# Optimization experiments

Hardware: AMD Instinct MI355X
Metric: run time of the kernel (lower is better)

The kernel has to match this reference:

```python
import jax, jax.numpy as jnp
import numpy as np

SEQ, BATCH, HIDDEN = 4096, 16, 512


def setup_inputs() -> dict:
    key = jax.random.key(0)
    ks = jax.random.split(key, 8)
    scale = 1.0 / np.sqrt(HIDDEN)
    outputs_hidden = jax.random.normal(ks[0], (1, BATCH, HIDDEN), jnp.float32)
    encoder_out = jax.random.normal(ks[1], (SEQ, BATCH, HIDDEN), jnp.float32)
    encoder_features = jax.random.normal(ks[2], (SEQ, BATCH, HIDDEN), jnp.float32)
    # binary-ish float mask, mostly ones
    encoder_mask = (jax.random.uniform(ks[3], (BATCH, 1, SEQ)) > 0.1).astype(jnp.float32)
    # running sum of positive exp-scores; keep strictly positive
    temporal_scores_sum = jax.random.uniform(ks[4], (BATCH, 1, SEQ)) + 0.5
    W_feat = jax.random.normal(ks[5], (HIDDEN, HIDDEN), jnp.float32) * scale
    b_feat = jax.random.normal(ks[6], (HIDDEN,), jnp.float32)
    v_attn = jax.random.normal(ks[7], (HIDDEN,), jnp.float32) * scale
    return {
        "outputs_hidden": outputs_hidden,
        "encoder_out": encoder_out,
        "encoder_features": encoder_features,
        "encoder_mask": encoder_mask,
        "temporal_scores_sum": temporal_scores_sum,
        "W_feat": W_feat,
        "b_feat": b_feat,
        "v_attn": v_attn,
    }


def reference(outputs_hidden, encoder_out, encoder_features, encoder_mask,
              temporal_scores_sum, W_feat, b_feat, v_attn):
    # self.features: Linear(hidden, hidden) on decoder state [1, b, h]
    decoder_features = jnp.einsum('obh,kh->obk', outputs_hidden, W_feat) + b_feat
    # additive score: tanh(dec + enc) . v  -> [s, b]
    scores = jnp.einsum('sbh,h->sb', jnp.tanh(decoder_features + encoder_features), v_attn)
    # Permute(1,2,0) of [s,b,1] -> [b,1,s], then exp
    temporal_attention = jnp.exp(scores).T[:, None, :]  # [b, 1, s]
    attention = temporal_attention / temporal_scores_sum
    new_scores_sum = temporal_attention + temporal_scores_sum
    attention = attention * encoder_mask
    attention = attention / jnp.sum(attention, axis=-1, keepdims=True)  # Normalize(-1)
    enc = jnp.transpose(encoder_out, (1, 0, 2))           # [b, s, h]
    context = jnp.matmul(attention, enc)                  # [b, 1, h]
    context = jnp.transpose(context, (1, 0, 2))           # [1, b, h]
    return context, attention, new_scores_sum
```

## Files before the change

kernel.cpp:

```cpp
#include <hip/hip_runtime.h>
#include <hip/hip_bf16.h>
#include <stdint.h>

#define SEQ 4096
#define BATCH 16
#define HID 512
#define ATT_OFF (BATCH * HID)
#define NSS_OFF (BATCH * HID + BATCH * SEQ)

#define SPW 2
#define NT 4
#define SBLK (4 * NT * SPW)
#define NGRP (SEQ / SBLK)
#define NBLK (BATCH * NGRP)

typedef unsigned short u16;
typedef unsigned int u32;

__device__ __forceinline__ float bflo(u32 w) { return __uint_as_float(w << 16); }
__device__ __forceinline__ float bfhi(u32 w) { return __uint_as_float(w & 0xffff0000u); }

__device__ __forceinline__ u16 f2bf(float f) {
  u32 u = __float_as_uint(f);
  return (u16)((u + 0x7fffu + ((u >> 16) & 1u)) >> 16);
}

__device__ __forceinline__ int probe_bf16(const void* tssp) {
  const u16* t = (const u16*)tssp;
  int ok = 1;
  #pragma unroll
  for (int i = 0; i < 8; i += 2) {
    u16 u = t[i];
    ok &= (u >= 0x3F00 && u <= 0x3FC0) ? 1 : 0;
  }
  return ok;
}

template <int BF>
__device__ __forceinline__ float ld1(const void* p, size_t i) {
  if (BF) return __uint_as_float(((u32)((const u16*)p)[i]) << 16);
  return ((const float*)p)[i];
}

template <int BF>
__device__ __forceinline__ void st1(void* p, size_t i, float v) {
  if (BF) ((u16*)p)[i] = f2bf(v);
  else    ((float*)p)[i] = v;
}

template <int BF>
__device__ __forceinline__ void load8(const void* p, size_t e, float* o) {
  if (BF) {
    uint4 v = *(const uint4*)((const u16*)p + e);
    o[0]=bflo(v.x); o[1]=bfhi(v.x); o[2]=bflo(v.y); o[3]=bfhi(v.y);
    o[4]=bflo(v.z); o[5]=bfhi(v.z); o[6]=bflo(v.w); o[7]=bfhi(v.w);
  } else {
    const float4* f = (const float4*)((const float*)p + e);
    float4 a = f[0], b = f[1];
    o[0]=a.x; o[1]=a.y; o[2]=a.z; o[3]=a.w;
    o[4]=b.x; o[5]=b.y; o[6]=b.z; o[7]=b.w;
  }
}

__device__ __forceinline__ float fast_tanh(float x) {
  float e = __expf(2.0f * x);
  return 1.0f - 2.0f * __builtin_amdgcn_rcpf(e + 1.0f);
}

template <int BF>
__device__ __forceinline__ void k_dec_body(
    const void* oh, const void* W, const void* bias, float* dec) {
  int tid = threadIdx.x;
  int gw = blockIdx.x * 4 + (tid >> 6);
  int lane = tid & 63;
  int k = gw & (HID - 1);
  int b = gw >> 9;
  float wv[8], ov[8];
  load8<BF>(W,  (size_t)k * HID + lane * 8, wv);
  load8<BF>(oh, (size_t)b * HID + lane * 8, ov);
  float acc = 0.0f;
  #pragma unroll
  for (int j = 0; j < 8; ++j) acc += wv[j] * ov[j];
  #pragma unroll
  for (int off = 32; off; off >>= 1) acc += __shfl_xor(acc, off, 64);
  if (lane == 0) dec[b * HID + k] = acc + ld1<BF>(bias, k);
}

__global__ __launch_bounds__(256) void k_dec(
    const void* oh, const void* W, const void* bias, const void* tss,
    float* dec, float* denom) {
  if (blockIdx.x == 0 && threadIdx.x < BATCH) denom[threadIdx.x] = 0.0f;
  if (probe_bf16(tss)) k_dec_body<1>(oh, W, bias, dec);
  else                 k_dec_body<0>(oh, W, bias, dec);
}

template <int BF>
__device__ __forceinline__ void k_str_body(
    const void* ef, const void* eo, const void* maskp, const void* tssp,
    const void* vp, const float* dec, float* w_buf, float* denom,
    float* partial, void* out) {
  int tid = threadIdx.x, lane = tid & 63, wave = tid >> 6;
  int blk = blockIdx.x;
  int b = blk & (BATCH - 1);
  int grp = blk >> 4;
  int sw = grp * SBLK + wave * (NT * SPW);

  float dv[8], vv[8];
  #pragma unroll
  for (int j = 0; j < 8; ++j) dv[j] = dec[b * HID + lane * 8 + j];
  load8<BF>(vp, lane * 8, vv);

  float evA[SPW][8], evB[SPW][8], eoA[SPW][8], eoB[SPW][8];
  float tsA[SPW], tsB[SPW], mA[SPW], mB[SPW];
  float a[8] = {0,0,0,0,0,0,0,0};
  float wsum = 0.0f;

  auto LOADT = [&](float (&ev)[SPW][8], float (&eov)[SPW][8],
                   float (&ts)[SPW], float (&m)[SPW], int t) {
    int s0 = sw + t * SPW;
    #pragma unroll
    for (int i = 0; i < SPW; ++i) {
      size_t row = ((size_t)(s0 + i) * BATCH + b) * HID + lane * 8;
      load8<BF>(ef, row, ev[i]);
      load8<BF>(eo, row, eov[i]);
    }
    #pragma unroll
    for (int i = 0; i < SPW; ++i) {
      ts[i] = ld1<BF>(tssp,  b * SEQ + s0 + i);
      m[i]  = ld1<BF>(maskp, b * SEQ + s0 + i);
    }
  };
  auto COMPT = [&](float (&ev)[SPW][8], float (&eov)[SPW][8],
                   float (&ts)[SPW], float (&m)[SPW], int t) {
    int s0 = sw + t * SPW;
    float acc[SPW];
    #pragma unroll
    for (int i = 0; i < SPW; ++i) {
      float s = 0.0f;
      #pragma unroll
      for (int j = 0; j < 8; ++j) s += fast_tanh(ev[i][j] + dv[j]) * vv[j];
      acc[i] = s;
    }
    #pragma unroll
    for (int off = 32; off; off >>= 1) {
      #pragma unroll
      for (int i = 0; i < SPW; ++i) acc[i] += __shfl_xor(acc[i], off, 64);
    }
    #pragma unroll
    for (int i = 0; i < SPW; ++i) {
      float p  = __expf(acc[i]);
      float wv = p * m[i] * __builtin_amdgcn_rcpf(ts[i]);
      wsum += wv;
      if (lane == 0) {
        st1<BF>(out, NSS_OFF + b * SEQ + s0 + i, p + ts[i]);
        w_buf[b * SEQ + s0 + i] = wv;
      }
      #pragma unroll
      for (int j = 0; j < 8; ++j) a[j] += wv * eov[i][j];
    }
  };

  LOADT(evA, eoA, tsA, mA, 0);
  LOADT(evB, eoB, tsB, mB, 1);
  COMPT(evA, eoA, tsA, mA, 0);  LOADT(evA, eoA, tsA, mA, 2);
  COMPT(evB, eoB, tsB, mB, 1);  LOADT(evB, eoB, tsB, mB, 3);
  COMPT(evA, eoA, tsA, mA, 2);
  COMPT(evB, eoB, tsB, mB, 3);

  __shared__ float red[3 * 8 * 64];
  __shared__ float wpart[4];
  if (lane == 0) wpart[wave] = wsum;
  if (wave > 0) {
    #pragma unroll
    for (int j = 0; j < 8; ++j) red[((wave - 1) * 8 + j) * 64 + lane] = a[j];
  }
  __syncthreads();
  if (wave == 0) {
    #pragma unroll
    for (int k = 0; k < 3; ++k)
      #pragma unroll
      for (int j = 0; j < 8; ++j) a[j] += red[(k * 8 + j) * 64 + lane];
    float4* p4 = (float4*)(partial + ((size_t)b * NGRP + grp) * HID + lane * 8);
    p4[0] = make_float4(a[0], a[1], a[2], a[3]);
    p4[1] = make_float4(a[4], a[5], a[6], a[7]);
    if (tid == 0)
      atomicAdd(&denom[b], wpart[0] + wpart[1] + wpart[2] + wpart[3]);
  }
}

__global__ __launch_bounds__(256, 3) void k_str(
    const void* ef, const void* eo, const void* maskp, const void* tssp,
    const void* vp, const float* dec, float* w_buf, float* denom,
    float* partial, void* out) {
  if (probe_bf16(tssp))
    k_str_body<1>(ef, eo, maskp, tssp, vp, dec, w_buf, denom, partial, out);
  else
    k_str_body<0>(ef, eo, maskp, tssp, vp, dec, w_buf, denom, partial, out);
}

template <int BF>
__device__ __forceinline__ void k_fin_body(
    const float* w_buf, const float* denom, const float* partial, void* out) {
  int b = blockIdx.x >> 5;
  int part = blockIdx.x & 31;
  int t = threadIdx.x;
  float inv_d = __builtin_amdgcn_rcpf(denom[b]);
  if (t < 128) {
    int s = part * 128 + t;
    st1<BF>(out, ATT_OFF + b * SEQ + s, w_buf[b * SEQ + s] * inv_d);
  }
  int hl = t >> 4, cp = t & 15;
  int h = part * 16 + hl;
  float sum = 0.0f;
  #pragma unroll
  for (int c = cp; c < NGRP; c += 16)
    sum += partial[((size_t)b * NGRP + c) * HID + h];
  #pragma unroll
  for (int off = 8; off; off >>= 1) sum += __shfl_xor(sum, off, 64);
  if (cp == 0) st1<BF>(out, b * HID + h, sum * inv_d);
}

__global__ __launch_bounds__(256) void k_finalize(
    const float* w_buf, const float* denom, const float* partial,
    const void* tssp, void* out) {
  if (probe_bf16(tssp)) k_fin_body<1>(w_buf, denom, partial, out);
  else                  k_fin_body<0>(w_buf, denom, partial, out);
}

extern "C" void kernel_launch(void* const* d_in, const int* in_sizes, int n_in,
                              void* d_out, int out_size, void* d_ws, size_t ws_size,
                              hipStream_t stream) {
  const void* oh   = d_in[0];
  const void* eo   = d_in[1];
  const void* ef   = d_in[2];
  const void* mask = d_in[3];
  const void* tss  = d_in[4];
  const void* W    = d_in[5];
  const void* bias = d_in[6];
  const void* v    = d_in[7];

  float* ws      = (float*)d_ws;
  float* dec     = ws;
  float* w_buf   = dec + BATCH * HID;
  float* denom   = w_buf + BATCH * SEQ;
  float* partial = denom + 16;

  k_dec     <<<2048, 256, 0, stream>>>(oh, W, bias, tss, dec, denom);
  k_str     <<<NBLK, 256, 0, stream>>>(ef, eo, mask, tss, v, dec, w_buf,
                                       denom, partial, d_out);
  k_finalize<<< 512, 256, 0, stream>>>(w_buf, denom, partial, tss, d_out);
}
```

Measured before the change: 293.8 us.

## Replace register double-buffered streaming with simple loop and raise occupancy

Removes the manual two-slot software pipelining of encoder rows in the streaming kernel and uses a plain non-unrolled loop over 8 sequence positions per wave. Register pressure drops, so the launch bound asks for 8 blocks per CU instead of 3, relying on more resident waves to hide memory latency instead of explicit prefetch. The per-block sequence chunk shrinks from 32 to 32 rows (same SBLK), so the grid and the partial layout stay unchanged. The risk is less memory-level parallelism per wave if the scheduler cannot cover the load latency.

```diff
diff --git a/kernel.cpp b/kernel.cpp
--- a/kernel.cpp
+++ b/kernel.cpp
@@ -8,9 +8,8 @@
 #define ATT_OFF (BATCH * HID)
 #define NSS_OFF (BATCH * HID + BATCH * SEQ)
 
-#define SPW 2
-#define NT 4
-#define SBLK (4 * NT * SPW)
+#define NT 8
+#define SBLK (4 * NT)
 #define NGRP (SEQ / SBLK)
 #define NBLK (BATCH * NGRP)
 
@@ -103,69 +102,40 @@
   int blk = blockIdx.x;
   int b = blk & (BATCH - 1);
   int grp = blk >> 4;
-  int sw = grp * SBLK + wave * (NT * SPW);
+  int sw = grp * SBLK + wave * NT;
 
   float dv[8], vv[8];
   #pragma unroll
   for (int j = 0; j < 8; ++j) dv[j] = dec[b * HID + lane * 8 + j];
   load8<BF>(vp, lane * 8, vv);
 
-  float evA[SPW][8], evB[SPW][8], eoA[SPW][8], eoB[SPW][8];
-  float tsA[SPW], tsB[SPW], mA[SPW], mB[SPW];
   float a[8] = {0,0,0,0,0,0,0,0};
   float wsum = 0.0f;
 
-  auto LOADT = [&](float (&ev)[SPW][8], float (&eov)[SPW][8],
-                   float (&ts)[SPW], float (&m)[SPW], int t) {
-    int s0 = sw + t * SPW;
-    #pragma unroll
-    for (int i = 0; i < SPW; ++i) {
-      size_t row = ((size_t)(s0 + i) * BATCH + b) * HID + lane * 8;
-      load8<BF>(ef, row, ev[i]);
-      load8<BF>(eo, row, eov[i]);
+  #pragma unroll 1
+  for (int t = 0; t < NT; ++t) {
+    int s = sw + t;
+    size_t row = ((size_t)s * BATCH + b) * HID + lane * 8;
+    float ev[8], eov[8];
+    load8<BF>(ef, row, ev);
+    load8<BF>(eo, row, eov);
+    float ts = ld1<BF>(tssp,  b * SEQ + s);
+    float m  = ld1<BF>(maskp, b * SEQ + s);
+    float acc = 0.0f;
+    #pragma unroll
+    for (int j = 0; j < 8; ++j) acc += fast_tanh(ev[j] + dv[j]) * vv[j];
+    #pragma unroll
+    for (int off = 32; off; off >>= 1) acc += __shfl_xor(acc, off, 64);
+    float p  = __expf(acc);
+    float wv = p * m * __builtin_amdgcn_rcpf(ts);
+    wsum += wv;
+    if (lane == 0) {
+      st1<BF>(out, NSS_OFF + b * SEQ + s, p + ts);
+      w_buf[b * SEQ + s] = wv;
     }
     #pragma unroll
-    for (int i = 0; i < SPW; ++i) {
-      ts[i] = ld1<BF>(tssp,  b * SEQ + s0 + i);
-      m[i]  = ld1<BF>(maskp, b * SEQ + s0 + i);
-    }
-  };
-  auto COMPT = [&](float (&ev)[SPW][8], float (&eov)[SPW][8],
-                   float (&ts)[SPW], float (&m)[SPW], int t) {
-    int s0 = sw + t * SPW;
-    float acc[SPW];
-    #pragma unroll
-    for (int i = 0; i < SPW; ++i) {
-      float s = 0.0f;
-      #pragma unroll
-      for (int j = 0; j < 8; ++j) s += fast_tanh(ev[i][j] + dv[j]) * vv[j];
-      acc[i] = s;
-    }
-    #pragma unroll
-    for (int off = 32; off; off >>= 1) {
-      #pragma unroll
-      for (int i = 0; i < SPW; ++i) acc[i] += __shfl_xor(acc[i], off, 64);
-    }
-    #pragma unroll
-    for (int i = 0; i < SPW; ++i) {
-      float p  = __expf(acc[i]);
-      float wv = p * m[i] * __builtin_amdgcn_rcpf(ts[i]);
-      wsum += wv;
-      if (lane == 0) {
-        st1<BF>(out, NSS_OFF + b * SEQ + s0 + i, p + ts[i]);
-        w_buf[b * SEQ + s0 + i] = wv;
-      }
-      #pragma unroll
-      for (int j = 0; j < 8; ++j) a[j] += wv * eov[i][j];
-    }
-  };
-
-  LOADT(evA, eoA, tsA, mA, 0);
-  LOADT(evB, eoB, tsB, mB, 1);
-  COMPT(evA, eoA, tsA, mA, 0);  LOADT(evA, eoA, tsA, mA, 2);
-  COMPT(evB, eoB, tsB, mB, 1);  LOADT(evB, eoB, tsB, mB, 3);
-  COMPT(evA, eoA, tsA, mA, 2);
-  COMPT(evB, eoB, tsB, mB, 3);
+    for (int j = 0; j < 8; ++j) a[j] += wv * eov[j];
+  }
 
   __shared__ float red[3 * 8 * 64];
   __shared__ float wpart[4];
@@ -188,7 +158,7 @@
   }
 }
 
-__global__ __launch_bounds__(256, 3) void k_str(
+__global__ __launch_bounds__(256, 8) void k_str(
     const void* ef, const void* eo, const void* maskp, const void* tssp,
     const void* vp, const float* dec, float* w_buf, float* denom,
     float* partial, void* out) {
```

New measurement: 303.7 us. +3.4%, slower.
